# Optimization experiments

Hardware: AMD Instinct MI355X
Metric: run time of the kernel (lower is better)

The kernel has to match this reference:

```python
import jax, jax.numpy as jnp
import numpy as np

TEMPERATURE = 0.07


def setup_inputs() -> dict:
    key = jax.random.key(0)
    k1, k2 = jax.random.split(key)
    B, D = 8192, 256
    embeddings = jax.random.normal(k1, (B, D), dtype=jnp.float32)
    ids = jax.random.randint(k2, (B,), 0, 1024, dtype=jnp.int64 if jax.config.jax_enable_x64 else jnp.int32)
    return {"embeddings": embeddings, "ids": ids}


def reference(embeddings, ids):
    B = embeddings.shape[0]
    # L2-normalize rows (F.normalize with p=2, dim=1)
    emb = embeddings / jnp.maximum(jnp.linalg.norm(embeddings, axis=1, keepdims=True), 1e-12)
    sim = (emb @ emb.T) / TEMPERATURE                      # [B, B]
    eye = jnp.eye(B, dtype=bool)
    sim = jnp.where(eye, -jnp.inf, sim)
    exp_sim = jnp.exp(sim)                                  # diag -> 0
    pos_mask = (ids[:, None] == ids[None, :]) & ~eye        # [B, B]
    pos_sum = jnp.sum(jnp.where(pos_mask, exp_sim, 0.0), axis=1)  # [B]
    all_sum = jnp.sum(exp_sim, axis=1)                      # [B]
    valid = pos_mask.any(axis=1)
    per_row = -jnp.log(pos_sum / all_sum)
    loss = jnp.sum(jnp.where(valid, per_row, 0.0))
    n_valid = jnp.sum(valid.astype(jnp.float32))
    return loss / jnp.maximum(n_valid, 1.0)
```

## Files before the change

kernel.cpp:

```cpp
#include <hip/hip_runtime.h>
#include <hip/hip_bf16.h>

#define B_SZ 8192
#define D_SZ 256
#define NTILES 2080
#define PRESCALE 4.539816004686735f

typedef __attribute__((ext_vector_type(4))) float f32x4;
typedef __attribute__((ext_vector_type(8))) short s16x8;

__device__ __forceinline__ void async_copy16(const void* g, void* l) {
    __builtin_amdgcn_global_load_lds(
        (const __attribute__((address_space(1))) unsigned int*)g,
        (__attribute__((address_space(3))) unsigned int*)l,
        16, 0, 0);
}

__global__ __launch_bounds__(256) void norm_kernel(const float* __restrict__ emb,
                                                   ushort* __restrict__ nbf,
                                                   float* __restrict__ sums) {
    const int wave = threadIdx.x >> 6, lane = threadIdx.x & 63;
    sums[blockIdx.x * 64 + (threadIdx.x >> 2) ] = 0.0f;

    for (int g = blockIdx.x; g < B_SZ / 4; g += 256) {
        const int row = g * 4 + wave;
        const float4 v = ((const float4*)(emb + (size_t)row * D_SZ))[lane];
        float ss = v.x * v.x + v.y * v.y + v.z * v.z + v.w * v.w;
        #pragma unroll
        for (int m = 1; m < 64; m <<= 1) ss += __shfl_xor(ss, m, 64);
        float s = PRESCALE / fmaxf(sqrtf(ss), 1e-12f);
        __hip_bfloat16 b0 = __float2bfloat16(v.x * s);
        __hip_bfloat16 b1 = __float2bfloat16(v.y * s);
        __hip_bfloat16 b2 = __float2bfloat16(v.z * s);
        __hip_bfloat16 b3 = __float2bfloat16(v.w * s);
        ushort4 o;
        o.x = *(ushort*)&b0; o.y = *(ushort*)&b1; o.z = *(ushort*)&b2; o.w = *(ushort*)&b3;
        ((ushort4*)(nbf + (size_t)row * D_SZ))[lane] = o;
    }
}

__global__ __launch_bounds__(256) void sim_kernel(const ushort* __restrict__ N,
                                                  const int* __restrict__ ids,
                                                  float* __restrict__ all_sum,
                                                  float* __restrict__ pos_sum) {
    __shared__ ushort sA[128 * 64];
    __shared__ ushort sB[128 * 64];

    const int t    = threadIdx.x;
    const int wave = t >> 6, lane = t & 63;
    const int wy   = wave >> 1, wx = wave & 1;
    const int r    = lane >> 3;
    const int c8s  = ((lane & 7) ^ r) * 8;
    const int myc  = lane & 15;

    for (int tb = blockIdx.x; tb < NTILES; tb += (int)gridDim.x) {
        int bj = (int)((sqrtf(8.0f * tb + 1.0f) - 1.0f) * 0.5f);
        while ((bj + 1) * (bj + 2) / 2 <= tb) ++bj;
        while (bj * (bj + 1) / 2 > tb) --bj;
        const int bi   = tb - bj * (bj + 1) / 2;
        const int i0   = bi * 128;
        const int j0   = bj * 128;
        const bool diag = (bi == bj);

        f32x4 acc[4][4];
        #pragma unroll
        for (int mi = 0; mi < 4; ++mi)
            #pragma unroll
            for (int ni = 0; ni < 4; ++ni)
                acc[mi][ni] = (f32x4){0.f, 0.f, 0.f, 0.f};

        for (int kk = 0; kk < 4; ++kk) {
            const int k0 = kk * 64;
            const ushort* gA = N + (size_t)(i0 + wave * 32) * D_SZ + k0;
            const ushort* gB = N + (size_t)(j0 + wave * 32) * D_SZ + k0;
            #pragma unroll
            for (int q = 0; q < 4; ++q) {
                async_copy16(gA + (size_t)(q * 8 + r) * D_SZ + c8s, &sA[(wave * 32 + q * 8) * 64]);
                async_copy16(gB + (size_t)(q * 8 + r) * D_SZ + c8s, &sB[(wave * 32 + q * 8) * 64]);
            }
            __syncthreads();

            #pragma unroll
            for (int ks = 0; ks < 2; ++ks) {
                const int C = ks * 4 + (lane >> 4);
                const int slot = (C ^ (lane & 7)) * 8;
                s16x8 af[4], bf[4];
                #pragma unroll
                for (int mi = 0; mi < 4; ++mi)
                    af[mi] = *(const s16x8*)&sA[(wy * 64 + mi * 16 + (lane & 15)) * 64 + slot];
                #pragma unroll
                for (int ni = 0; ni < 4; ++ni)
                    bf[ni] = *(const s16x8*)&sB[(wx * 64 + ni * 16 + (lane & 15)) * 64 + slot];
                #pragma unroll
                for (int mi = 0; mi < 4; ++mi)
                    #pragma unroll
                    for (int ni = 0; ni < 4; ++ni)
                        acc[mi][ni] = __builtin_amdgcn_mfma_f32_16x16x32_bf16(
                            af[mi], bf[ni], acc[mi][ni], 0, 0, 0);
            }
            __syncthreads();
        }

        float* rowAllPart = (float*)sA;
        float* rowPosPart = (float*)sB;

        int idc[4];
        #pragma unroll
        for (int ni = 0; ni < 4; ++ni)
            idc[ni] = ids[j0 + wx * 64 + ni * 16 + myc];

        float cAll[4] = {0.f, 0.f, 0.f, 0.f};
        float cPos[4] = {0.f, 0.f, 0.f, 0.f};

        #pragma unroll
        for (int mi = 0; mi < 4; ++mi) {
            float rAll[4] = {0.f, 0.f, 0.f, 0.f};
            float rPos[4] = {0.f, 0.f, 0.f, 0.f};
            const int rbase = wy * 64 + mi * 16 + (lane >> 4) * 4;
            const int4 idr  = *(const int4*)&ids[i0 + rbase];
            #pragma unroll
            for (int ni = 0; ni < 4; ++ni) {
                const int cloc = wx * 64 + ni * 16 + myc;
                #pragma unroll
                for (int rg = 0; rg < 4; ++rg) {
                    const int lr = rbase + rg;
                    float e = __builtin_amdgcn_exp2f(acc[mi][ni][rg]);
                    if (diag && lr == cloc) e = 0.0f;
                    rAll[rg] += e; cAll[ni] += e;
                    const int idrv = (rg == 0) ? idr.x : (rg == 1) ? idr.y
                                   : (rg == 2) ? idr.z : idr.w;
                    if (idrv == idc[ni]) { rPos[rg] += e; cPos[ni] += e; }
                }
            }
            #pragma unroll
            for (int rg = 0; rg < 4; ++rg) {
                rowAllPart[(rbase + rg) * 32 + wx * 16 + myc] = rAll[rg];
                rowPosPart[(rbase + rg) * 32 + wx * 16 + myc] = rPos[rg];
            }
        }

        if (!diag) {
            #pragma unroll
            for (int ni = 0; ni < 4; ++ni) {
                cAll[ni] += __shfl_xor(cAll[ni], 16, 64);
                cAll[ni] += __shfl_xor(cAll[ni], 32, 64);
                cPos[ni] += __shfl_xor(cPos[ni], 16, 64);
                cPos[ni] += __shfl_xor(cPos[ni], 32, 64);
            }
            if (lane < 16) {
                #pragma unroll
                for (int ni = 0; ni < 4; ++ni) {
                    const int gc = j0 + wx * 64 + ni * 16 + lane;
                    atomicAdd(&all_sum[gc], cAll[ni]);
                    atomicAdd(&pos_sum[gc], cPos[ni]);
                }
            }
        }

        __syncthreads();
        {
            const int row = t & 127;
            const float* src = (t >= 128) ? rowPosPart : rowAllPart;
            float s = 0.0f;
            #pragma unroll
            for (int k8 = 0; k8 < 8; ++k8) {
                const int chunk = (k8 + (row & 7)) & 7;
                const float4 v = *(const float4*)&src[row * 32 + chunk * 4];
                s += v.x + v.y + v.z + v.w;
            }
            float* dst = (t >= 128) ? pos_sum : all_sum;
            atomicAdd(&dst[i0 + row], s);
        }
        __syncthreads();
    }
}

__global__ __launch_bounds__(256) void loss_kernel(const float* __restrict__ all_sum,
                                                   const float* __restrict__ pos_sum,
                                                   float* __restrict__ out) {
    float loss = 0.0f, cnt = 0.0f;
    for (int i = threadIdx.x; i < B_SZ; i += 256) {
        float p = pos_sum[i], a = all_sum[i];
        if (p > 0.0f) { loss += logf(a) - logf(p); cnt += 1.0f; }
    }
    #pragma unroll
    for (int m = 1; m < 64; m <<= 1) {
        loss += __shfl_xor(loss, m, 64);
        cnt  += __shfl_xor(cnt, m, 64);
    }
    __shared__ float sl[4], sc[4];
    int wave = threadIdx.x >> 6, lane = threadIdx.x & 63;
    if (lane == 0) { sl[wave] = loss; sc[wave] = cnt; }
    __syncthreads();
    if (threadIdx.x == 0) {
        float L = sl[0] + sl[1] + sl[2] + sl[3];
        float C = sc[0] + sc[1] + sc[2] + sc[3];
        out[0] = L / fmaxf(C, 1.0f);
    }
}

extern "C" void kernel_launch(void* const* d_in, const int* in_sizes, int n_in,
                              void* d_out, int out_size, void* d_ws, size_t ws_size,
                              hipStream_t stream) {
    const float* emb = (const float*)d_in[0];
    const int*   ids = (const int*)d_in[1];
    float*       out = (float*)d_out;

    float*  all_sum = (float*)d_ws;
    float*  pos_sum = all_sum + B_SZ;
    ushort* nbf     = (ushort*)((char*)d_ws + 65536);

    norm_kernel<<<256, 256, 0, stream>>>(emb, nbf, all_sum);
    sim_kernel<<<1024, 256, 0, stream>>>(nbf, ids, all_sum, pos_sum);
    loss_kernel<<<1, 256, 0, stream>>>(all_sum, pos_sum, out);
}
```

Measured before the change: 124.0 us.

## Compute positive sums via sparse id matching and prefetch next tile stage

The masked positive-pair sum is moved out of the dense 128x128 tile epilogue. Each wave now scans the ids with ballots and computes dot products only for matching rows, writing pos_sum directly. The tile loop issues the first K-stage of the next tile before the exp/reduction epilogue so the load overlaps with it. Row sums now use cross-lane shuffles and atomics instead of an LDS staging pass with an extra barrier. The trade-offs are a serial ballot scan of 8192 ids per row, more global atomics, and positive sums computed in fp32 from bf16 rather than from the MFMA results.

```diff
diff --git a/kernel.cpp b/kernel.cpp
--- a/kernel.cpp
+++ b/kernel.cpp
@@ -4,6 +4,7 @@
 #define B_SZ 8192
 #define D_SZ 256
 #define NTILES 2080
+#define GRID_SIM 1024
 #define PRESCALE 4.539816004686735f
 
 typedef __attribute__((ext_vector_type(4))) float f32x4;
@@ -16,12 +17,16 @@
         16, 0, 0);
 }
 
+__device__ __forceinline__ float bf16_as_f32(unsigned u) {
+    return __uint_as_float(u << 16);
+}
+
 __global__ __launch_bounds__(256) void norm_kernel(const float* __restrict__ emb,
                                                    ushort* __restrict__ nbf,
-                                                   float* __restrict__ sums) {
+                                                   float* __restrict__ all_sum) {
+    if (threadIdx.x < 32) all_sum[blockIdx.x * 32 + threadIdx.x] = 0.0f;
+
     const int wave = threadIdx.x >> 6, lane = threadIdx.x & 63;
-    sums[blockIdx.x * 64 + (threadIdx.x >> 2) ] = 0.0f;
-
     for (int g = blockIdx.x; g < B_SZ / 4; g += 256) {
         const int row = g * 4 + wave;
         const float4 v = ((const float4*)(emb + (size_t)row * D_SZ))[lane];
@@ -39,6 +44,27 @@
     }
 }
 
+__device__ __forceinline__ void decode_tile(int tb, int& i0, int& j0, bool& diag) {
+    int bj = (int)((sqrtf(8.0f * tb + 1.0f) - 1.0f) * 0.5f);
+    while ((bj + 1) * (bj + 2) / 2 <= tb) ++bj;
+    while (bj * (bj + 1) / 2 > tb) --bj;
+    const int bi = tb - bj * (bj + 1) / 2;
+    i0 = bi * 128; j0 = bj * 128; diag = (bi == bj);
+}
+
+__device__ __forceinline__ void issue_stage(const ushort* __restrict__ N,
+                                            int i0, int j0, int k0,
+                                            ushort* sA, ushort* sB,
+                                            int wave, int r, int c8s) {
+    const ushort* gA = N + (size_t)(i0 + wave * 32) * D_SZ + k0;
+    const ushort* gB = N + (size_t)(j0 + wave * 32) * D_SZ + k0;
+    #pragma unroll
+    for (int q = 0; q < 4; ++q) {
+        async_copy16(gA + (size_t)(q * 8 + r) * D_SZ + c8s, &sA[(wave * 32 + q * 8) * 64]);
+        async_copy16(gB + (size_t)(q * 8 + r) * D_SZ + c8s, &sB[(wave * 32 + q * 8) * 64]);
+    }
+}
+
 __global__ __launch_bounds__(256) void sim_kernel(const ushort* __restrict__ N,
                                                   const int* __restrict__ ids,
                                                   float* __restrict__ all_sum,
@@ -53,15 +79,35 @@
     const int c8s  = ((lane & 7) ^ r) * 8;
     const int myc  = lane & 15;
 
-    for (int tb = blockIdx.x; tb < NTILES; tb += (int)gridDim.x) {
-        int bj = (int)((sqrtf(8.0f * tb + 1.0f) - 1.0f) * 0.5f);
-        while ((bj + 1) * (bj + 2) / 2 <= tb) ++bj;
-        while (bj * (bj + 1) / 2 > tb) --bj;
-        const int bi   = tb - bj * (bj + 1) / 2;
-        const int i0   = bi * 128;
-        const int j0   = bj * 128;
-        const bool diag = (bi == bj);
-
+    int tb = blockIdx.x;
+    int i0, j0; bool diag;
+    decode_tile(tb, i0, j0, diag);
+    issue_stage(N, i0, j0, 0, sA, sB, wave, r, c8s);
+
+    for (int i = blockIdx.x * 4 + wave; i < B_SZ; i += GRID_SIM * 4) {
+        const int idi = ids[i];
+        const ushort4 u = *(const ushort4*)&N[(size_t)i * D_SZ + lane * 4];
+        const float a0 = bf16_as_f32(u.x), a1 = bf16_as_f32(u.y);
+        const float a2 = bf16_as_f32(u.z), a3 = bf16_as_f32(u.w);
+        float s = 0.0f;
+        for (int base = 0; base < B_SZ; base += 64) {
+            unsigned long long m = __ballot(ids[base + lane] == idi);
+            if (i >= base && i < base + 64) m &= ~(1ull << (i - base));
+            while (m) {
+                const int j = base + __ffsll(m) - 1;
+                m &= m - 1;
+                const ushort4 w = *(const ushort4*)&N[(size_t)j * D_SZ + lane * 4];
+                float d = a0 * bf16_as_f32(w.x) + a1 * bf16_as_f32(w.y)
+                        + a2 * bf16_as_f32(w.z) + a3 * bf16_as_f32(w.w);
+                #pragma unroll
+                for (int mm = 1; mm < 64; mm <<= 1) d += __shfl_xor(d, mm, 64);
+                s += __builtin_amdgcn_exp2f(d);
+            }
+        }
+        if (lane == 0) pos_sum[i] = s;
+    }
+
+    while (true) {
         f32x4 acc[4][4];
         #pragma unroll
         for (int mi = 0; mi < 4; ++mi)
@@ -70,16 +116,7 @@
                 acc[mi][ni] = (f32x4){0.f, 0.f, 0.f, 0.f};
 
         for (int kk = 0; kk < 4; ++kk) {
-            const int k0 = kk * 64;
-            const ushort* gA = N + (size_t)(i0 + wave * 32) * D_SZ + k0;
-            const ushort* gB = N + (size_t)(j0 + wave * 32) * D_SZ + k0;
-            #pragma unroll
-            for (int q = 0; q < 4; ++q) {
-                async_copy16(gA + (size_t)(q * 8 + r) * D_SZ + c8s, &sA[(wave * 32 + q * 8) * 64]);
-                async_copy16(gB + (size_t)(q * 8 + r) * D_SZ + c8s, &sB[(wave * 32 + q * 8) * 64]);
-            }
             __syncthreads();
-
             #pragma unroll
             for (int ks = 0; ks < 2; ++ks) {
                 const int C = ks * 4 + (lane >> 4);
@@ -99,79 +136,58 @@
                             af[mi], bf[ni], acc[mi][ni], 0, 0, 0);
             }
             __syncthreads();
-        }
-
-        float* rowAllPart = (float*)sA;
-        float* rowPosPart = (float*)sB;
-
-        int idc[4];
-        #pragma unroll
-        for (int ni = 0; ni < 4; ++ni)
-            idc[ni] = ids[j0 + wx * 64 + ni * 16 + myc];
+            if (kk < 3) issue_stage(N, i0, j0, (kk + 1) * 64, sA, sB, wave, r, c8s);
+        }
+
+        const int ntb = tb + GRID_SIM;
+        int ni0 = 0, nj0 = 0; bool ndiag = false;
+        if (ntb < NTILES) {
+            decode_tile(ntb, ni0, nj0, ndiag);
+            issue_stage(N, ni0, nj0, 0, sA, sB, wave, r, c8s);
+        }
 
         float cAll[4] = {0.f, 0.f, 0.f, 0.f};
-        float cPos[4] = {0.f, 0.f, 0.f, 0.f};
-
         #pragma unroll
         for (int mi = 0; mi < 4; ++mi) {
             float rAll[4] = {0.f, 0.f, 0.f, 0.f};
-            float rPos[4] = {0.f, 0.f, 0.f, 0.f};
             const int rbase = wy * 64 + mi * 16 + (lane >> 4) * 4;
-            const int4 idr  = *(const int4*)&ids[i0 + rbase];
             #pragma unroll
             for (int ni = 0; ni < 4; ++ni) {
                 const int cloc = wx * 64 + ni * 16 + myc;
                 #pragma unroll
                 for (int rg = 0; rg < 4; ++rg) {
-                    const int lr = rbase + rg;
                     float e = __builtin_amdgcn_exp2f(acc[mi][ni][rg]);
-                    if (diag && lr == cloc) e = 0.0f;
+                    if (diag && (rbase + rg) == cloc) e = 0.0f;
                     rAll[rg] += e; cAll[ni] += e;
-                    const int idrv = (rg == 0) ? idr.x : (rg == 1) ? idr.y
-                                   : (rg == 2) ? idr.z : idr.w;
-                    if (idrv == idc[ni]) { rPos[rg] += e; cPos[ni] += e; }
                 }
             }
             #pragma unroll
             for (int rg = 0; rg < 4; ++rg) {
-                rowAllPart[(rbase + rg) * 32 + wx * 16 + myc] = rAll[rg];
-                rowPosPart[(rbase + rg) * 32 + wx * 16 + myc] = rPos[rg];
-            }
-        }
-
+                #pragma unroll
+                for (int mm = 1; mm < 16; mm <<= 1)
+                    rAll[rg] += __shfl_xor(rAll[rg], mm, 64);
+            }
+            if (myc == 0) {
+                #pragma unroll
+                for (int rg = 0; rg < 4; ++rg)
+                    atomicAdd(&all_sum[i0 + rbase + rg], rAll[rg]);
+            }
+        }
         if (!diag) {
             #pragma unroll
             for (int ni = 0; ni < 4; ++ni) {
                 cAll[ni] += __shfl_xor(cAll[ni], 16, 64);
                 cAll[ni] += __shfl_xor(cAll[ni], 32, 64);
-                cPos[ni] += __shfl_xor(cPos[ni], 16, 64);
-                cPos[ni] += __shfl_xor(cPos[ni], 32, 64);
             }
             if (lane < 16) {
                 #pragma unroll
-                for (int ni = 0; ni < 4; ++ni) {
-                    const int gc = j0 + wx * 64 + ni * 16 + lane;
-                    atomicAdd(&all_sum[gc], cAll[ni]);
-                    atomicAdd(&pos_sum[gc], cPos[ni]);
-                }
-            }
-        }
-
-        __syncthreads();
-        {
-            const int row = t & 127;
-            const float* src = (t >= 128) ? rowPosPart : rowAllPart;
-            float s = 0.0f;
-            #pragma unroll
-            for (int k8 = 0; k8 < 8; ++k8) {
-                const int chunk = (k8 + (row & 7)) & 7;
-                const float4 v = *(const float4*)&src[row * 32 + chunk * 4];
-                s += v.x + v.y + v.z + v.w;
-            }
-            float* dst = (t >= 128) ? pos_sum : all_sum;
-            atomicAdd(&dst[i0 + row], s);
-        }
-        __syncthreads();
+                for (int ni = 0; ni < 4; ++ni)
+                    atomicAdd(&all_sum[j0 + wx * 64 + ni * 16 + lane], cAll[ni]);
+            }
+        }
+
+        if (ntb >= NTILES) break;
+        tb = ntb; i0 = ni0; j0 = nj0; diag = ndiag;
     }
 }
 
@@ -211,6 +227,6 @@
     ushort* nbf     = (ushort*)((char*)d_ws + 65536);
 
     norm_kernel<<<256, 256, 0, stream>>>(emb, nbf, all_sum);
-    sim_kernel<<<1024, 256, 0, stream>>>(nbf, ids, all_sum, pos_sum);
+    sim_kernel<<<GRID_SIM, 256, 0, stream>>>(nbf, ids, all_sum, pos_sum);
     loss_kernel<<<1, 256, 0, stream>>>(all_sum, pos_sum, out);
 }
```

After: 218.0 us. +75.9%, slower.

## Widen sim tiles to 128x256 with new symmetric tile decode and shuffle-based row reduction

Applied to the files above, without the earlier changes.

Each workgroup now computes a 128x256 block of the similarity matrix, doubling the MFMA accumulators per wave, and covers the symmetric upper triangle with a new tile decode. On the diagonal blocks it masks the lower-or-equal part, since those pairs are handled elsewhere. Row sums are reduced with wave shuffles and sent with atomics instead of the LDS partial buffer and extra barrier, and zero positive sums skip their atomics. The grid shrinks to 512 blocks. This raises operand reuse and cuts tile count, at the cost of more registers, less occupancy, and some wasted compute on the masked halves of diagonal tiles.

```diff
diff --git a/kernel.cpp b/kernel.cpp
--- a/kernel.cpp
+++ b/kernel.cpp
@@ -3,7 +3,8 @@
 
 #define B_SZ 8192
 #define D_SZ 256
-#define NTILES 2080
+#define NTILES2 1056
+#define GRID_SIM 512
 #define PRESCALE 4.539816004686735f
 
 typedef __attribute__((ext_vector_type(4))) float f32x4;
@@ -19,9 +20,9 @@
 __global__ __launch_bounds__(256) void norm_kernel(const float* __restrict__ emb,
                                                    ushort* __restrict__ nbf,
                                                    float* __restrict__ sums) {
+    sums[blockIdx.x * 64 + (threadIdx.x >> 2)] = 0.0f;
+
     const int wave = threadIdx.x >> 6, lane = threadIdx.x & 63;
-    sums[blockIdx.x * 64 + (threadIdx.x >> 2) ] = 0.0f;
-
     for (int g = blockIdx.x; g < B_SZ / 4; g += 256) {
         const int row = g * 4 + wave;
         const float4 v = ((const float4*)(emb + (size_t)row * D_SZ))[lane];
@@ -39,12 +40,20 @@
     }
 }
 
+__device__ __forceinline__ void decode_tile2(int tb, int& i0, int& j0, bool& masked) {
+    int bi = 0, off = 0;
+    while (off + (32 - (bi >> 1)) <= tb) { off += 32 - (bi >> 1); ++bi; }
+    const int bj2 = (bi >> 1) + (tb - off);
+    i0 = bi * 128; j0 = bj2 * 256;
+    masked = (bj2 == (bi >> 1));
+}
+
 __global__ __launch_bounds__(256) void sim_kernel(const ushort* __restrict__ N,
                                                   const int* __restrict__ ids,
                                                   float* __restrict__ all_sum,
                                                   float* __restrict__ pos_sum) {
     __shared__ ushort sA[128 * 64];
-    __shared__ ushort sB[128 * 64];
+    __shared__ ushort sB[256 * 64];
 
     const int t    = threadIdx.x;
     const int wave = t >> 6, lane = t & 63;
@@ -53,79 +62,73 @@
     const int c8s  = ((lane & 7) ^ r) * 8;
     const int myc  = lane & 15;
 
-    for (int tb = blockIdx.x; tb < NTILES; tb += (int)gridDim.x) {
-        int bj = (int)((sqrtf(8.0f * tb + 1.0f) - 1.0f) * 0.5f);
-        while ((bj + 1) * (bj + 2) / 2 <= tb) ++bj;
-        while (bj * (bj + 1) / 2 > tb) --bj;
-        const int bi   = tb - bj * (bj + 1) / 2;
-        const int i0   = bi * 128;
-        const int j0   = bj * 128;
-        const bool diag = (bi == bj);
-
-        f32x4 acc[4][4];
+    for (int tb = blockIdx.x; tb < NTILES2; tb += GRID_SIM) {
+        int i0, j0; bool masked;
+        decode_tile2(tb, i0, j0, masked);
+
+        f32x4 acc[4][8];
         #pragma unroll
         for (int mi = 0; mi < 4; ++mi)
             #pragma unroll
-            for (int ni = 0; ni < 4; ++ni)
+            for (int ni = 0; ni < 8; ++ni)
                 acc[mi][ni] = (f32x4){0.f, 0.f, 0.f, 0.f};
 
         for (int kk = 0; kk < 4; ++kk) {
             const int k0 = kk * 64;
             const ushort* gA = N + (size_t)(i0 + wave * 32) * D_SZ + k0;
-            const ushort* gB = N + (size_t)(j0 + wave * 32) * D_SZ + k0;
-            #pragma unroll
-            for (int q = 0; q < 4; ++q) {
+            const ushort* gB = N + (size_t)(j0 + wave * 64) * D_SZ + k0;
+            #pragma unroll
+            for (int q = 0; q < 4; ++q)
                 async_copy16(gA + (size_t)(q * 8 + r) * D_SZ + c8s, &sA[(wave * 32 + q * 8) * 64]);
-                async_copy16(gB + (size_t)(q * 8 + r) * D_SZ + c8s, &sB[(wave * 32 + q * 8) * 64]);
-            }
+            #pragma unroll
+            for (int q = 0; q < 8; ++q)
+                async_copy16(gB + (size_t)(q * 8 + r) * D_SZ + c8s, &sB[(wave * 64 + q * 8) * 64]);
             __syncthreads();
 
             #pragma unroll
             for (int ks = 0; ks < 2; ++ks) {
                 const int C = ks * 4 + (lane >> 4);
                 const int slot = (C ^ (lane & 7)) * 8;
-                s16x8 af[4], bf[4];
+                s16x8 af[4], bf[8];
                 #pragma unroll
                 for (int mi = 0; mi < 4; ++mi)
                     af[mi] = *(const s16x8*)&sA[(wy * 64 + mi * 16 + (lane & 15)) * 64 + slot];
                 #pragma unroll
-                for (int ni = 0; ni < 4; ++ni)
-                    bf[ni] = *(const s16x8*)&sB[(wx * 64 + ni * 16 + (lane & 15)) * 64 + slot];
+                for (int ni = 0; ni < 8; ++ni)
+                    bf[ni] = *(const s16x8*)&sB[(wx * 128 + ni * 16 + (lane & 15)) * 64 + slot];
                 #pragma unroll
                 for (int mi = 0; mi < 4; ++mi)
                     #pragma unroll
-                    for (int ni = 0; ni < 4; ++ni)
+                    for (int ni = 0; ni < 8; ++ni)
                         acc[mi][ni] = __builtin_amdgcn_mfma_f32_16x16x32_bf16(
                             af[mi], bf[ni], acc[mi][ni], 0, 0, 0);
             }
             __syncthreads();
         }
 
-        float* rowAllPart = (float*)sA;
-        float* rowPosPart = (float*)sB;
-
-        int idc[4];
-        #pragma unroll
-        for (int ni = 0; ni < 4; ++ni)
-            idc[ni] = ids[j0 + wx * 64 + ni * 16 + myc];
-
-        float cAll[4] = {0.f, 0.f, 0.f, 0.f};
-        float cPos[4] = {0.f, 0.f, 0.f, 0.f};
+        const int R0 = i0 + wy * 64;
+        const int CB = j0 + wx * 128;
+        int idc[8];
+        #pragma unroll
+        for (int ni = 0; ni < 8; ++ni)
+            idc[ni] = ids[CB + ni * 16 + myc];
+
+        float cAll[8] = {0.f,0.f,0.f,0.f,0.f,0.f,0.f,0.f};
+        float cPos[8] = {0.f,0.f,0.f,0.f,0.f,0.f,0.f,0.f};
 
         #pragma unroll
         for (int mi = 0; mi < 4; ++mi) {
+            const int rbl = mi * 16 + (lane >> 4) * 4;
+            const int4 idr = *(const int4*)&ids[R0 + rbl];
             float rAll[4] = {0.f, 0.f, 0.f, 0.f};
             float rPos[4] = {0.f, 0.f, 0.f, 0.f};
-            const int rbase = wy * 64 + mi * 16 + (lane >> 4) * 4;
-            const int4 idr  = *(const int4*)&ids[i0 + rbase];
-            #pragma unroll
-            for (int ni = 0; ni < 4; ++ni) {
-                const int cloc = wx * 64 + ni * 16 + myc;
+            #pragma unroll
+            for (int ni = 0; ni < 8; ++ni) {
+                const int gj = CB + ni * 16 + myc;
                 #pragma unroll
                 for (int rg = 0; rg < 4; ++rg) {
-                    const int lr = rbase + rg;
                     float e = __builtin_amdgcn_exp2f(acc[mi][ni][rg]);
-                    if (diag && lr == cloc) e = 0.0f;
+                    if (masked && (R0 + rbl + rg) >= gj) e = 0.0f;
                     rAll[rg] += e; cAll[ni] += e;
                     const int idrv = (rg == 0) ? idr.x : (rg == 1) ? idr.y
                                    : (rg == 2) ? idr.z : idr.w;
@@ -134,42 +137,34 @@
             }
             #pragma unroll
             for (int rg = 0; rg < 4; ++rg) {
-                rowAllPart[(rbase + rg) * 32 + wx * 16 + myc] = rAll[rg];
-                rowPosPart[(rbase + rg) * 32 + wx * 16 + myc] = rPos[rg];
-            }
-        }
-
-        if (!diag) {
-            #pragma unroll
-            for (int ni = 0; ni < 4; ++ni) {
-                cAll[ni] += __shfl_xor(cAll[ni], 16, 64);
-                cAll[ni] += __shfl_xor(cAll[ni], 32, 64);
-                cPos[ni] += __shfl_xor(cPos[ni], 16, 64);
-                cPos[ni] += __shfl_xor(cPos[ni], 32, 64);
-            }
-            if (lane < 16) {
-                #pragma unroll
-                for (int ni = 0; ni < 4; ++ni) {
-                    const int gc = j0 + wx * 64 + ni * 16 + lane;
-                    atomicAdd(&all_sum[gc], cAll[ni]);
-                    atomicAdd(&pos_sum[gc], cPos[ni]);
+                #pragma unroll
+                for (int mm = 1; mm < 16; mm <<= 1) {
+                    rAll[rg] += __shfl_xor(rAll[rg], mm, 64);
+                    rPos[rg] += __shfl_xor(rPos[rg], mm, 64);
                 }
             }
-        }
-
-        __syncthreads();
-        {
-            const int row = t & 127;
-            const float* src = (t >= 128) ? rowPosPart : rowAllPart;
-            float s = 0.0f;
-            #pragma unroll
-            for (int k8 = 0; k8 < 8; ++k8) {
-                const int chunk = (k8 + (row & 7)) & 7;
-                const float4 v = *(const float4*)&src[row * 32 + chunk * 4];
-                s += v.x + v.y + v.z + v.w;
-            }
-            float* dst = (t >= 128) ? pos_sum : all_sum;
-            atomicAdd(&dst[i0 + row], s);
+            if (myc == 0) {
+                #pragma unroll
+                for (int rg = 0; rg < 4; ++rg) {
+                    atomicAdd(&all_sum[R0 + rbl + rg], rAll[rg]);
+                    if (rPos[rg] != 0.0f) atomicAdd(&pos_sum[R0 + rbl + rg], rPos[rg]);
+                }
+            }
+        }
+
+        #pragma unroll
+        for (int ni = 0; ni < 8; ++ni) {
+            cAll[ni] += __shfl_xor(cAll[ni], 16, 64);
+            cAll[ni] += __shfl_xor(cAll[ni], 32, 64);
+            cPos[ni] += __shfl_xor(cPos[ni], 16, 64);
+            cPos[ni] += __shfl_xor(cPos[ni], 32, 64);
+        }
+        if (lane < 16) {
+            #pragma unroll
+            for (int ni = 0; ni < 8; ++ni) {
+                atomicAdd(&all_sum[CB + ni * 16 + lane], cAll[ni]);
+                if (cPos[ni] != 0.0f) atomicAdd(&pos_sum[CB + ni * 16 + lane], cPos[ni]);
+            }
         }
         __syncthreads();
     }
@@ -211,6 +206,6 @@
     ushort* nbf     = (ushort*)((char*)d_ws + 65536);
 
     norm_kernel<<<256, 256, 0, stream>>>(emb, nbf, all_sum);
-    sim_kernel<<<1024, 256, 0, stream>>>(nbf, ids, all_sum, pos_sum);
+    sim_kernel<<<GRID_SIM, 256, 0, stream>>>(nbf, ids, all_sum, pos_sum);
     loss_kernel<<<1, 256, 0, stream>>>(all_sum, pos_sum, out);
 }
```

New measurement: 152.1 us. +22.7%, slower.

## Software-pipeline sim kernel with register prefetch and double-buffered LDS

Applied to the files above, without the earlier changes.

Replaces the direct global-to-LDS async copies with register-staged loads. The next K-slice, or the next tile's first slice, is fetched into registers while the current slice is computed, and LDS is double-buffered so one barrier per K step is removed. The grid is halved to 512 persistent blocks so each block loops over more tiles and can prefetch across them, and zero positive-sum atomics are skipped. In exchange the kernel uses more registers and twice the LDS (64KB), which can lower occupancy, and a smaller grid may leave some CUs underused.

```diff
diff --git a/kernel.cpp b/kernel.cpp
--- a/kernel.cpp
+++ b/kernel.cpp
@@ -4,24 +4,18 @@
 #define B_SZ 8192
 #define D_SZ 256
 #define NTILES 2080
+#define GRID_SIM 512
 #define PRESCALE 4.539816004686735f
 
 typedef __attribute__((ext_vector_type(4))) float f32x4;
 typedef __attribute__((ext_vector_type(8))) short s16x8;
-
-__device__ __forceinline__ void async_copy16(const void* g, void* l) {
-    __builtin_amdgcn_global_load_lds(
-        (const __attribute__((address_space(1))) unsigned int*)g,
-        (__attribute__((address_space(3))) unsigned int*)l,
-        16, 0, 0);
-}
 
 __global__ __launch_bounds__(256) void norm_kernel(const float* __restrict__ emb,
                                                    ushort* __restrict__ nbf,
                                                    float* __restrict__ sums) {
+    sums[blockIdx.x * 64 + (threadIdx.x >> 2)] = 0.0f;
+
     const int wave = threadIdx.x >> 6, lane = threadIdx.x & 63;
-    sums[blockIdx.x * 64 + (threadIdx.x >> 2) ] = 0.0f;
-
     for (int g = blockIdx.x; g < B_SZ / 4; g += 256) {
         const int row = g * 4 + wave;
         const float4 v = ((const float4*)(emb + (size_t)row * D_SZ))[lane];
@@ -39,12 +33,42 @@
     }
 }
 
+__device__ __forceinline__ void decode_tile(int tb, int& i0, int& j0, bool& diag) {
+    int bj = (int)((sqrtf(8.0f * tb + 1.0f) - 1.0f) * 0.5f);
+    while ((bj + 1) * (bj + 2) / 2 <= tb) ++bj;
+    while (bj * (bj + 1) / 2 > tb) --bj;
+    const int bi = tb - bj * (bj + 1) / 2;
+    i0 = bi * 128; j0 = bj * 128; diag = (bi == bj);
+}
+
+__device__ __forceinline__ void load_regs(s16x8 ra[4], s16x8 rb[4],
+                                          const ushort* __restrict__ N,
+                                          int i0, int j0, int k0,
+                                          int wave, int r, int c8s) {
+    const ushort* gA = N + (size_t)(i0 + wave * 32) * D_SZ + k0;
+    const ushort* gB = N + (size_t)(j0 + wave * 32) * D_SZ + k0;
+    #pragma unroll
+    for (int q = 0; q < 4; ++q) {
+        ra[q] = *(const s16x8*)(gA + (size_t)(q * 8 + r) * D_SZ + c8s);
+        rb[q] = *(const s16x8*)(gB + (size_t)(q * 8 + r) * D_SZ + c8s);
+    }
+}
+
+__device__ __forceinline__ void store_stage(const s16x8 ra[4], const s16x8 rb[4],
+                                            ushort* bA, ushort* bB,
+                                            int wave, int lane) {
+    #pragma unroll
+    for (int q = 0; q < 4; ++q) {
+        *(s16x8*)&bA[(wave * 32 + q * 8) * 64 + lane * 8] = ra[q];
+        *(s16x8*)&bB[(wave * 32 + q * 8) * 64 + lane * 8] = rb[q];
+    }
+}
+
 __global__ __launch_bounds__(256) void sim_kernel(const ushort* __restrict__ N,
                                                   const int* __restrict__ ids,
                                                   float* __restrict__ all_sum,
                                                   float* __restrict__ pos_sum) {
-    __shared__ ushort sA[128 * 64];
-    __shared__ ushort sB[128 * 64];
+    __shared__ ushort smem[4 * 128 * 64];
 
     const int t    = threadIdx.x;
     const int wave = t >> 6, lane = t & 63;
@@ -53,14 +77,18 @@
     const int c8s  = ((lane & 7) ^ r) * 8;
     const int myc  = lane & 15;
 
-    for (int tb = blockIdx.x; tb < NTILES; tb += (int)gridDim.x) {
-        int bj = (int)((sqrtf(8.0f * tb + 1.0f) - 1.0f) * 0.5f);
-        while ((bj + 1) * (bj + 2) / 2 <= tb) ++bj;
-        while (bj * (bj + 1) / 2 > tb) --bj;
-        const int bi   = tb - bj * (bj + 1) / 2;
-        const int i0   = bi * 128;
-        const int j0   = bj * 128;
-        const bool diag = (bi == bj);
+    int tb = blockIdx.x;
+    int i0, j0; bool diag;
+    decode_tile(tb, i0, j0, diag);
+
+    s16x8 ra[4], rb[4];
+    load_regs(ra, rb, N, i0, j0, 0, wave, r, c8s);
+
+    while (true) {
+        const int ntb = tb + GRID_SIM;
+        const bool have_next = (ntb < NTILES);
+        int ni0 = i0, nj0 = j0; bool ndiag = diag;
+        if (have_next) decode_tile(ntb, ni0, nj0, ndiag);
 
         f32x4 acc[4][4];
         #pragma unroll
@@ -69,15 +97,13 @@
             for (int ni = 0; ni < 4; ++ni)
                 acc[mi][ni] = (f32x4){0.f, 0.f, 0.f, 0.f};
 
+        #pragma unroll
         for (int kk = 0; kk < 4; ++kk) {
-            const int k0 = kk * 64;
-            const ushort* gA = N + (size_t)(i0 + wave * 32) * D_SZ + k0;
-            const ushort* gB = N + (size_t)(j0 + wave * 32) * D_SZ + k0;
-            #pragma unroll
-            for (int q = 0; q < 4; ++q) {
-                async_copy16(gA + (size_t)(q * 8 + r) * D_SZ + c8s, &sA[(wave * 32 + q * 8) * 64]);
-                async_copy16(gB + (size_t)(q * 8 + r) * D_SZ + c8s, &sB[(wave * 32 + q * 8) * 64]);
-            }
+            ushort* bA = smem + (kk & 1) * 16384;
+            ushort* bB = bA + 8192;
+            store_stage(ra, rb, bA, bB, wave, lane);
+            if (kk < 3)           load_regs(ra, rb, N, i0, j0, (kk + 1) * 64, wave, r, c8s);
+            else if (have_next)   load_regs(ra, rb, N, ni0, nj0, 0, wave, r, c8s);
             __syncthreads();
 
             #pragma unroll
@@ -87,10 +113,10 @@
                 s16x8 af[4], bf[4];
                 #pragma unroll
                 for (int mi = 0; mi < 4; ++mi)
-                    af[mi] = *(const s16x8*)&sA[(wy * 64 + mi * 16 + (lane & 15)) * 64 + slot];
+                    af[mi] = *(const s16x8*)&bA[(wy * 64 + mi * 16 + (lane & 15)) * 64 + slot];
                 #pragma unroll
                 for (int ni = 0; ni < 4; ++ni)
-                    bf[ni] = *(const s16x8*)&sB[(wx * 64 + ni * 16 + (lane & 15)) * 64 + slot];
+                    bf[ni] = *(const s16x8*)&bB[(wx * 64 + ni * 16 + (lane & 15)) * 64 + slot];
                 #pragma unroll
                 for (int mi = 0; mi < 4; ++mi)
                     #pragma unroll
@@ -98,11 +124,10 @@
                         acc[mi][ni] = __builtin_amdgcn_mfma_f32_16x16x32_bf16(
                             af[mi], bf[ni], acc[mi][ni], 0, 0, 0);
             }
-            __syncthreads();
-        }
-
-        float* rowAllPart = (float*)sA;
-        float* rowPosPart = (float*)sB;
+        }
+
+        float* rowAllPart = (float*)smem;
+        float* rowPosPart = (float*)&smem[8192];
 
         int idc[4];
         #pragma unroll
@@ -152,7 +177,7 @@
                 for (int ni = 0; ni < 4; ++ni) {
                     const int gc = j0 + wx * 64 + ni * 16 + lane;
                     atomicAdd(&all_sum[gc], cAll[ni]);
-                    atomicAdd(&pos_sum[gc], cPos[ni]);
+                    if (cPos[ni] != 0.0f) atomicAdd(&pos_sum[gc], cPos[ni]);
                 }
             }
         }
@@ -172,6 +197,9 @@
             atomicAdd(&dst[i0 + row], s);
         }
         __syncthreads();
+
+        if (!have_next) break;
+        tb = ntb; i0 = ni0; j0 = nj0; diag = ndiag;
     }
 }
 
@@ -211,6 +239,6 @@
     ushort* nbf     = (ushort*)((char*)d_ws + 65536);
 
     norm_kernel<<<256, 256, 0, stream>>>(emb, nbf, all_sum);
-    sim_kernel<<<1024, 256, 0, stream>>>(nbf, ids, all_sum, pos_sum);
+    sim_kernel<<<GRID_SIM, 256, 0, stream>>>(nbf, ids, all_sum, pos_sum);
     loss_kernel<<<1, 256, 0, stream>>>(all_sum, pos_sum, out);
 }
```

New measurement: 117.4 us (median of 2 runs). 1.06x faster.
